# Kernel optimization log

Hardware: AMD Instinct MI355X
Metric: run time of the kernel (lower is better)

Reference implementation:

```python
import jax, jax.numpy as jnp
from jax import lax
import numpy as np

B, N, D = 64, 1025, 384   # tokens = 1 CLS + 32x32 patch grid
G = 32
K = 8                      # num rotation bases
KS = 8                     # num scale bases
R = 8                      # rank of skew bases
H = 128                    # controller hidden dim
CIN = 3 * D                # cls_mean_var pooling
OUT = D
ROT_GATE_BIAS = -4.0
LOCAL_GATE_BIAS = -3.0


def setup_inputs() -> dict:
    key = jax.random.key(0)
    ks = jax.random.split(key, 16)
    f32 = jnp.float32
    inp = {
        "x": jax.random.normal(ks[0], (B, N, D), f32),
        "shared_weight": jax.random.normal(ks[1], (OUT, D), f32) * 0.02,
        "bias": jnp.zeros((OUT,), f32),
        "left_basis": jax.random.normal(ks[2], (K, D, R), f32) * 0.02,
        "right_basis": jax.random.normal(ks[3], (K, D, R), f32) * 0.02,
        "scale_basis": jax.random.normal(ks[4], (KS, OUT), f32) * 0.01,
        "scale_strength": jnp.asarray(0.25, f32),
        "dw_kernel": jax.random.normal(ks[5], (D, 1, 3, 3), f32) * 0.1,  # depthwise 3x3
        "ctrl_w1": jax.random.normal(ks[6], (H, CIN), f32) * 0.02,
        "ctrl_b1": jnp.zeros((H,), f32),
        "w_rot": jax.random.normal(ks[7], (K, H), f32) * 0.02,
        "b_rot": jnp.zeros((K,), f32),
        "w_rgate": jax.random.normal(ks[8], (1, H), f32) * 0.02,
        "b_rgate": jnp.full((1,), ROT_GATE_BIAS, f32),
        "w_lgate": jax.random.normal(ks[9], (1, H), f32) * 0.02,
        "b_lgate": jnp.full((1,), LOCAL_GATE_BIAS, f32),
        "w_scale": jax.random.normal(ks[10], (KS, H), f32) * 0.02,
        "b_scale": jnp.zeros((KS,), f32),
    }
    return inp


def _forward(x, shared_weight, bias, left_basis, right_basis, scale_basis,
             scale_strength, dw_kernel, ctrl_w1, ctrl_b1, w_rot, b_rot,
             w_rgate, b_rgate, w_lgate, b_lgate, w_scale, b_scale):
    b, n, d = x.shape
    # --- conditioning signal: cls | mean | var (unbiased=False) ---
    cls = x[:, 0]
    mean = jnp.mean(x, axis=1)
    var = jnp.var(x, axis=1)
    z = jnp.concatenate([cls, mean, var], axis=-1)          # [B, 3D]
    # --- controller MLP ---
    h = jax.nn.gelu(z @ ctrl_w1.T + ctrl_b1)                 # [B, H]
    rot_coeff = jnp.tanh(h @ w_rot.T + b_rot)                # [B, K]
    rot_gate = jax.nn.sigmoid(h @ w_rgate.T + b_rgate)[:, 0] # [B]
    local_gate = jax.nn.sigmoid(h @ w_lgate.T + b_lgate)[:, 0]
    scale_coeff = jnp.tanh(h @ w_scale.T + b_scale)          # [B, KS]
    # --- gated local depthwise-conv mixer on the patch grid ---
    cls_tok = x[:, :1, :]
    patch = x[:, 1:, :]                                      # [B, G*G, D]
    grid = patch.transpose(0, 2, 1).reshape(b, d, G, G)      # NCHW
    local = lax.conv_general_dilated(
        grid, dw_kernel, window_strides=(1, 1), padding="SAME",
        feature_group_count=d, dimension_numbers=("NCHW", "OIHW", "NCHW"))
    local_tok = local.reshape(b, d, G * G).transpose(0, 2, 1)
    mixed_patch = patch + local_gate[:, None, None] * (local_tok - patch)
    lm = jnp.concatenate([cls_tok, mixed_patch], axis=1)     # [B, N, D]
    # --- normalized skew bases from low-rank factors ---
    basis = (jnp.einsum("kdr,ker->kde", left_basis, right_basis)
             - jnp.einsum("kdr,ker->kde", right_basis, left_basis))  # [K, D, D]
    norm = jnp.maximum(jnp.linalg.norm(basis.reshape(K, -1), axis=1), 1e-6)
    basis = basis / norm[:, None, None]
    # --- per-sample Cayley rotation (fp32 solve) ---
    skew = jnp.einsum("bk,kde->bde", rot_coeff, basis)       # residual_scale = 1.0
    eye = jnp.eye(d, dtype=jnp.float32)
    half = 0.5 * skew
    transform = jnp.linalg.solve(eye - half, jnp.broadcast_to(eye, half.shape) + half)
    transform = transform.astype(x.dtype)
    # --- gated rotation of features ---
    rotated = jnp.einsum("bnd,bdh->bnh", lm, transform)
    mixed = lm + rot_gate[:, None, None] * (rotated - lm)
    # --- shared linear + dynamic output scaling ---
    preact = mixed @ shared_weight.T + bias                  # [B, N, OUT]
    scale_delta = jnp.tanh(scale_coeff @ scale_basis)        # [B, OUT]
    scale = 1.0 + scale_strength * scale_delta[:, None, :]
    return preact * scale


def reference(x, shared_weight, bias, left_basis, right_basis, scale_basis,
              scale_strength, dw_kernel, ctrl_w1, ctrl_b1, w_rot, b_rot,
              w_rgate, b_rgate, w_lgate, b_lgate, w_scale, b_scale):
    return _forward(x, shared_weight, bias, left_basis, right_basis, scale_basis,
                    scale_strength, dw_kernel, ctrl_w1, ctrl_b1, w_rot, b_rot,
                    w_rgate, b_rgate, w_lgate, b_lgate, w_scale, b_scale)
```

## Files before the change

kernel.cpp:

```cpp
#include <hip/hip_runtime.h>
#include <hip/hip_bf16.h>
#include <math.h>

static const int Bb = 64, Nn = 1025, Dd = 384, Kk = 8, Rr = 8, Hh = 128, CINc = 1152, OUTo = 384;

#define OFF_PSTAT 0u
#define OFF_RC    475136u
#define OFF_RG    475648u
#define OFF_LG    475712u
#define OFF_SCALE 476288u
#define OFF_N2    505472u
#define OFF_P     505600u
#define OFF_Q     554752u
#define OFF_G     603904u
#define OFF_QW    620288u
#define OFF_PB    669440u
#define OFF_EP    694016u
#define OFF_ZT    3839744u
#define OFF_WBT   5412608u
#define OFF_LM    10131200u

typedef __attribute__((ext_vector_type(8))) short short8;
typedef __attribute__((ext_vector_type(8))) __bf16 bf16x8;
typedef __attribute__((ext_vector_type(4))) float f32x4;

#define MFMA_BF16(a,b,c) __builtin_amdgcn_mfma_f32_16x16x32_bf16( \
    __builtin_bit_cast(bf16x8,(a)), __builtin_bit_cast(bf16x8,(b)), (c), 0, 0, 0)

#define GLDS16(gp, lp) __builtin_amdgcn_global_load_lds( \
    (__attribute__((address_space(1))) void*)(gp), \
    (__attribute__((address_space(3))) void*)(lp), 16, 0, 0)

__device__ __forceinline__ float gelu_t(float v){
    float u = 0.7978845608028654f*(v + 0.044715f*v*v*v);
    return 0.5f*v*(1.0f + tanhf(u));
}
__device__ __forceinline__ float sigm(float v){ return 1.0f/(1.0f+expf(-v)); }
__device__ __forceinline__ unsigned short f2bf(float v){
    return __builtin_bit_cast(unsigned short, __float2bfloat16(v));
}

__global__ __launch_bounds__(384) void k_statsprep(const float* __restrict__ x,
    const float* __restrict__ lb, const float* __restrict__ rb,
    float* __restrict__ ps, float* __restrict__ n2,
    float* __restrict__ P, float* __restrict__ Q, unsigned short* __restrict__ Pb){
    int bid = blockIdx.x, t = threadIdx.x;
    if (bid < 512){
        int s = bid & 7, b = bid >> 3;
        int dq = t % 96, ng = t / 96;
        int n0 = s*129, n1 = n0+129 < Nn ? n0+129 : Nn;
        const float4* xb = (const float4*)(x + (size_t)b*Nn*Dd);
        float4 sm = make_float4(0.f,0.f,0.f,0.f), sq = make_float4(0.f,0.f,0.f,0.f);
        for (int n = n0+ng; n < n1; n += 4){
            float4 v = xb[(size_t)n*96 + dq];
            sm.x += v.x; sm.y += v.y; sm.z += v.z; sm.w += v.w;
            sq.x += v.x*v.x; sq.y += v.y*v.y; sq.z += v.z*v.z; sq.w += v.w*v.w;
        }
        __shared__ float4 smS[384];
        __shared__ float4 sqS[384];
        smS[t] = sm; sqS[t] = sq;
        __syncthreads();
        if (t < 96){
            float4 a0 = smS[t], a1 = smS[t+96], a2 = smS[t+192], a3 = smS[t+288];
            float4 q0 = sqS[t], q1 = sqS[t+96], q2 = sqS[t+192], q3 = sqS[t+288];
            float4 a = make_float4(a0.x+a1.x+a2.x+a3.x, a0.y+a1.y+a2.y+a3.y, a0.z+a1.z+a2.z+a3.z, a0.w+a1.w+a2.w+a3.w);
            float4 q = make_float4(q0.x+q1.x+q2.x+q3.x, q0.y+q1.y+q2.y+q3.y, q0.z+q1.z+q2.z+q3.z, q0.w+q1.w+q2.w+q3.w);
            ((float4*)(ps + ((size_t)(b*8+s)*2+0)*Dd))[t] = a;
            ((float4*)(ps + ((size_t)(b*8+s)*2+1)*Dd))[t] = q;
        }
    } else if (bid < 520){
        if (t < 64){
            int k = bid - 512;
            int r = t >> 3, s2 = t & 7;
            const float* L = lb + (size_t)k*Dd*Rr;
            const float* R = rb + (size_t)k*Dd*Rr;
            float a = 0.f, bsum = 0.f, c = 0.f, c2 = 0.f;
            for (int d = 0; d < Dd; ++d){
                float lr = L[d*8+r], ls = L[d*8+s2], rr = R[d*8+r], rs = R[d*8+s2];
                a += lr*ls; bsum += rr*rs; c += lr*rs; c2 += ls*rr;
            }
            float contrib = a*bsum - c*c2;
            for (int m = 32; m > 0; m >>= 1) contrib += __shfl_xor(contrib, m, 64);
            if (t == 0) n2[k] = 2.f*contrib;
        }
    } else {
        int idx = (bid - 520)*384 + t;
        int d = idx >> 7, j = idx & 127;
        int k = (j & 63) >> 3, r = j & 7;
        float lv = lb[((size_t)k*Dd + d)*Rr + r];
        float rv = rb[((size_t)k*Dd + d)*Rr + r];
        float pv = (j < 64) ? lv : rv;
        P[idx] = pv;
        Pb[idx] = f2bf(pv);
        Q[idx] = (j < 64) ? rv : lv;
    }
}

__global__ __launch_bounds__(512) void k_ctrlgram(const float* __restrict__ x, const float* __restrict__ ps,
    const float* __restrict__ w1, const float* __restrict__ b1,
    const float* __restrict__ w_rot, const float* __restrict__ b_rot,
    const float* __restrict__ w_rg, const float* __restrict__ b_rg,
    const float* __restrict__ w_lg, const float* __restrict__ b_lg,
    const float* __restrict__ w_sc, const float* __restrict__ b_sc,
    const float* __restrict__ sbasis, const float* __restrict__ sstr,
    const float* __restrict__ P, const float* __restrict__ Q, const float* __restrict__ Wsh,
    float* __restrict__ rc, float* __restrict__ rg, float* __restrict__ lg,
    float* __restrict__ scalev, unsigned short* __restrict__ lm,
    float* __restrict__ G, float* __restrict__ QW){
    int bid = blockIdx.x, t = threadIdx.x;
    if (bid < 128){
        __shared__ float qc[384];
        int i = bid;
        for (int d = t; d < Dd; d += 512) qc[d] = Q[d*128 + i];
        __syncthreads();
        if (t < 128){
            float a = 0.f;
            for (int d = 0; d < Dd; ++d) a += qc[d]*P[d*128 + t];
            G[i*128 + t] = a;
        } else {
            int o = t - 128;
            float a = 0.f;
            const float* wrow = Wsh + (size_t)o*Dd;
            for (int d = 0; d < Dd; ++d) a += qc[d]*wrow[d];
            QW[(size_t)i*OUTo + o] = a;
        }
    } else {
        __shared__ float zs[1152];
        __shared__ float hp[4*128];
        __shared__ float hs[128];
        __shared__ float scl[8];
        int b = bid - 128;
        if (t < 384){
            float sm = 0.f, sq = 0.f;
            for (int s = 0; s < 8; ++s){
                sm += ps[((size_t)(b*8+s)*2+0)*Dd + t];
                sq += ps[((size_t)(b*8+s)*2+1)*Dd + t];
            }
            float mean = sm*(1.0f/Nn);
            float var  = sq*(1.0f/Nn) - mean*mean;
            float cls  = x[(size_t)b*Nn*Dd + t];
            zs[t] = cls; zs[Dd + t] = mean; zs[2*Dd + t] = var;
            lm[(size_t)b*Nn*Dd + t] = f2bf(cls);
        }
        __syncthreads();
        {
            int row = t & 127, part = t >> 7;
            const float* wrow = w1 + (size_t)row*CINc + part*288;
            const float* zp = zs + part*288;
            float acc = 0.f;
            for (int c = 0; c < 288; ++c) acc += zp[c]*wrow[c];
            hp[part*128 + row] = acc;
        }
        __syncthreads();
        if (t < 128)
            hs[t] = gelu_t(hp[t] + hp[128+t] + hp[256+t] + hp[384+t] + b1[t]);
        __syncthreads();
        if (t < 8){
            float acc = b_rot[t]; const float* w = w_rot + (size_t)t*Hh;
            for (int c = 0; c < Hh; ++c) acc += hs[c]*w[c];
            rc[b*8+t] = tanhf(acc);
        } else if (t == 8){
            float acc = b_rg[0];
            for (int c = 0; c < Hh; ++c) acc += hs[c]*w_rg[c];
            rg[b] = sigm(acc);
        } else if (t == 9){
            float acc = b_lg[0];
            for (int c = 0; c < Hh; ++c) acc += hs[c]*w_lg[c];
            lg[b] = sigm(acc);
        } else if (t < 18){
            int q = t-10; float acc = b_sc[q]; const float* w = w_sc + (size_t)q*Hh;
            for (int c = 0; c < Hh; ++c) acc += hs[c]*w[c];
            scl[q] = tanhf(acc);
        }
        __syncthreads();
        if (t < 384){
            float acc = 0.f;
            #pragma unroll
            for (int q = 0; q < 8; ++q) acc += scl[q]*sbasis[q*OUTo + t];
            scalev[(size_t)b*OUTo + t] = 1.0f + sstr[0]*tanhf(acc);
        }
    }
}

__global__ __launch_bounds__(512) void k_cayley(const float* __restrict__ G, const float* __restrict__ rc,
                                                const float* __restrict__ n2, const float* __restrict__ rg,
                                                float* __restrict__ Ep){
    __shared__ float GT[128*128];
    __shared__ float Xs[128*128];
    int b = blockIdx.x, t = threadIdx.x;
    for (int lin = t; lin < 16384; lin += 512){
        int i = lin >> 7, m = lin & 127;
        GT[m*128 + i] = G[lin];
    }
    int j0 = (t & 15)*8, i0 = (t >> 4)*4;
    float dj[8], di[4];
    #pragma unroll
    for (int u = 0; u < 8; ++u){
        int j = j0+u; int k = (j&63)>>3;
        float nrm = fmaxf(sqrtf(n2[k]), 1e-6f);
        float al = 0.5f*rc[b*8+k]/nrm;
        dj[u] = (j < 64) ? al : -al;
    }
    #pragma unroll
    for (int u = 0; u < 4; ++u){
        int i = i0+u; int k = (i&63)>>3;
        float nrm = fmaxf(sqrtf(n2[k]), 1e-6f);
        float al = 0.5f*rc[b*8+k]/nrm;
        di[u] = (i < 64) ? al : -al;
    }
    __syncthreads();
    float B0[4][8], acc[4][8];
    #pragma unroll
    for (int ui = 0; ui < 4; ++ui)
        #pragma unroll
        for (int uj = 0; uj < 8; ++uj){
            int i = i0+ui, j = j0+uj;
            float g = GT[j*128 + i];
            B0[ui][uj] = di[ui]*g*dj[uj] + ((i==j) ? di[ui] : 0.f);
        }
    #pragma unroll
    for (int ui = 0; ui < 4; ++ui)
        #pragma unroll
        for (int uj = 0; uj < 8; ++uj)
            Xs[(i0+ui)*128 + j0+uj] = B0[ui][uj];
    __syncthreads();
    for (int pass = 0; pass < 2; ++pass){
        #pragma unroll
        for (int ui = 0; ui < 4; ++ui)
            #pragma unroll
            for (int uj = 0; uj < 8; ++uj) acc[ui][uj] = 0.f;
        for (int m = 0; m < 128; ++m){
            float4 g4 = *(const float4*)&GT[m*128 + i0];
            float4 xa = *(const float4*)&Xs[m*128 + j0];
            float4 xb = *(const float4*)&Xs[m*128 + j0 + 4];
            float gi[4] = {g4.x, g4.y, g4.z, g4.w};
            float xv[8] = {xa.x, xa.y, xa.z, xa.w, xb.x, xb.y, xb.z, xb.w};
            #pragma unroll
            for (int ui = 0; ui < 4; ++ui)
                #pragma unroll
                for (int uj = 0; uj < 8; ++uj)
                    acc[ui][uj] += gi[ui]*xv[uj];
        }
        if (pass == 0){
            __syncthreads();
            #pragma unroll
            for (int ui = 0; ui < 4; ++ui)
                #pragma unroll
                for (int uj = 0; uj < 8; ++uj)
                    Xs[(i0+ui)*128 + j0+uj] = B0[ui][uj] + di[ui]*acc[ui][uj];
            __syncthreads();
        }
    }
    float rgb = rg[b];
    #pragma unroll
    for (int ui = 0; ui < 4; ++ui){
        int i = i0+ui;
        float o[8];
        #pragma unroll
        for (int uj = 0; uj < 8; ++uj){
            int j = j0+uj;
            float x2 = B0[ui][uj] + di[ui]*acc[ui][uj];
            o[uj] = rgb*(x2 + ((i==j) ? di[ui] : 0.f));
        }
        float4* ep4 = (float4*)(Ep + ((size_t)b*128 + i)*128 + j0);
        ep4[0] = make_float4(o[0], o[1], o[2], o[3]);
        ep4[1] = make_float4(o[4], o[5], o[6], o[7]);
    }
}

__global__ __launch_bounds__(384) void k_zmlm(const float* __restrict__ x, const float* __restrict__ kw,
    const float* __restrict__ lg, const float* __restrict__ Ep, const float* __restrict__ QW,
    unsigned short* __restrict__ lm, unsigned short* __restrict__ ZT){
    int bid = blockIdx.x, t = threadIdx.x;
    if (bid < 2048){
        __shared__ float kws[9*384];
        int flat = bid;
        int work = (flat & 7)*256 + (flat >> 3);
        int b = work >> 5, gy = work & 31;
        for (int i = t; i < 3456; i += 384){
            int d = i % 384, tap = i / 384;
            kws[tap*384 + d] = kw[d*9 + tap];
        }
        __syncthreads();
        int dq = t % 96, gxg = t / 96;
        float lgb = lg[b];
        const float4* xb = (const float4*)(x + (size_t)b*Nn*Dd);
        unsigned short* lmb = lm + (size_t)b*Nn*Dd;
        #pragma unroll
        for (int u = 0; u < 8; ++u){
            int gx = gxg + 4*u;
            int n = 1 + (gy << 5) + gx;
            float4 xc = xb[(size_t)n*96 + dq];
            float ax = 0.f, ay = 0.f, az = 0.f, aw = 0.f;
            #pragma unroll
            for (int ky = 0; ky < 3; ++ky){
                int yy = gy + ky - 1;
                if ((unsigned)yy < 32u){
                    #pragma unroll
                    for (int kx = 0; kx < 3; ++kx){
                        int xx = gx + kx - 1;
                        if ((unsigned)xx < 32u){
                            float4 xv = xb[(size_t)(1 + (yy << 5) + xx)*96 + dq];
                            const float4 kv = *(const float4*)(&kws[(ky*3+kx)*384 + dq*4]);
                            ax += xv.x*kv.x; ay += xv.y*kv.y; az += xv.z*kv.z; aw += xv.w*kv.w;
                        }
                    }
                }
            }
            ushort4 o4;
            o4.x = f2bf(xc.x + lgb*(ax - xc.x));
            o4.y = f2bf(xc.y + lgb*(ay - xc.y));
            o4.z = f2bf(xc.z + lgb*(az - xc.z));
            o4.w = f2bf(xc.w + lgb*(aw - xc.w));
            *(ushort4*)(lmb + (size_t)n*Dd + dq*4) = o4;
        }
    } else {
        __shared__ float Es[4*128];
        int z = bid - 2048;
        int ig = z & 31, b = z >> 5;
        int i0 = ig*4;
        for (int lin = t; lin < 512; lin += 384)
            Es[lin] = Ep[((size_t)b*128 + i0 + (lin >> 7))*128 + (lin & 127)];
        __syncthreads();
        float a0=0.f, a1=0.f, a2=0.f, a3=0.f;
        for (int m = 0; m < 128; ++m){
            float qw = QW[(size_t)m*OUTo + t];
            a0 += Es[m]*qw; a1 += Es[128+m]*qw; a2 += Es[256+m]*qw; a3 += Es[384+m]*qw;
        }
        ushort4 uv;
        uv.x = f2bf(a0); uv.y = f2bf(a1); uv.z = f2bf(a2); uv.w = f2bf(a3);
        *(ushort4*)(ZT + ((size_t)b*OUTo + t)*128 + i0) = uv;
    }
}

__global__ __launch_bounds__(256) void k_wbt(const unsigned short* __restrict__ ZT, const unsigned short* __restrict__ Pb,
                                             const float* __restrict__ Wsh, unsigned short* __restrict__ WbT){
    __shared__ short8 As[256];
    __shared__ short8 Bs[256];
    int b = blockIdx.y;
    int mt = blockIdx.x/6, nt2 = blockIdx.x%6;
    int m0 = mt*64, n0 = nt2*64;
    int t = threadIdx.x;
    int w = t>>6, l = t&63;
    int wr = w>>1, wc = w&1;
    const unsigned short* Ab = ZT + (size_t)b*OUTo*128;
    int lrow = t>>2, lseg = t&3;
    f32x4 acc[2][2];
    #pragma unroll
    for (int mi=0;mi<2;++mi)
        #pragma unroll
        for (int ni=0;ni<2;++ni)
            #pragma unroll
            for (int q=0;q<4;++q) acc[mi][ni][q] = 0.f;
    for (int kt = 0; kt < 4; ++kt){
        int k0 = kt*32;
        short8 av = *(const short8*)(Ab + (size_t)(m0+lrow)*128 + k0 + lseg*8);
        short8 bv = *(const short8*)(Pb + (size_t)(n0+lrow)*128 + k0 + lseg*8);
        __syncthreads();
        As[lseg*64 + lrow] = av;
        Bs[lseg*64 + lrow] = bv;
        __syncthreads();
        short8 a0 = As[(l>>4)*64 + wr*32 + (l&15)];
        short8 a1 = As[(l>>4)*64 + wr*32 + 16 + (l&15)];
        short8 b0 = Bs[(l>>4)*64 + wc*32 + (l&15)];
        short8 b1 = Bs[(l>>4)*64 + wc*32 + 16 + (l&15)];
        acc[0][0] = MFMA_BF16(a0, b0, acc[0][0]);
        acc[0][1] = MFMA_BF16(a0, b1, acc[0][1]);
        acc[1][0] = MFMA_BF16(a1, b0, acc[1][0]);
        acc[1][1] = MFMA_BF16(a1, b1, acc[1][1]);
    }
    unsigned short* Wo = WbT + (size_t)b*OUTo*Dd;
    #pragma unroll
    for (int mi=0;mi<2;++mi){
        #pragma unroll
        for (int ni=0;ni<2;++ni){
            int col = n0 + wc*32 + ni*16 + (l&15);
            #pragma unroll
            for (int r=0;r<4;++r){
                int row = m0 + wr*32 + mi*16 + (l>>4)*4 + r;
                float v = Wsh[(size_t)row*Dd + col] + acc[mi][ni][r];
                Wo[(size_t)row*Dd + col] = f2bf(v);
            }
        }
    }
}

__global__ __launch_bounds__(256) void k_gemm_nt(const unsigned short* __restrict__ lm, const unsigned short* __restrict__ WbT,
                                                 const float* __restrict__ bias, const float* __restrict__ scalev,
                                                 float* __restrict__ out){
    __shared__ unsigned short smem[32768];
    __shared__ float svs[128];
    __shared__ float bvs[128];
    int flat = blockIdx.x;
    int work = (flat & 7)*216 + (flat >> 3);
    int b = work / 27;
    int r = work - b*27;
    int nt = r / 3, ot = r - nt*3;
    int n0 = nt*128, o0 = ot*128;
    int t = threadIdx.x;
    int w = t >> 6, l = t & 63;
    int wr = w >> 1, wc = w & 1;
    const unsigned short* Ab = lm + (size_t)b*Nn*Dd;
    const unsigned short* Bt = WbT + (size_t)b*OUTo*Dd;
    if (t < 128){ svs[t] = scalev[(size_t)b*OUTo + o0 + t]; bvs[t] = bias[o0 + t]; }
    int srow = l >> 2;
    int gch  = (l & 3) ^ ((l >> 3) & 3);
    f32x4 acc[4][4];
    #pragma unroll
    for (int fi = 0; fi < 4; ++fi)
        #pragma unroll
        for (int fj = 0; fj < 4; ++fj)
            #pragma unroll
            for (int q = 0; q < 4; ++q) acc[fi][fj][q] = 0.f;

#define STG(bufi, k0) { \
    unsigned short* Adst = &smem[(bufi)*8192 + (w*32)*32]; \
    unsigned short* Bdst = &smem[(bufi)*8192 + 4096 + (w*32)*32]; \
    GLDS16(Ab + (size_t)(n0 + w*32 + srow)*Dd + (k0) + gch*8, Adst); \
    GLDS16(Ab + (size_t)(n0 + w*32 + 16 + srow)*Dd + (k0) + gch*8, Adst + 512); \
    GLDS16(Bt + (size_t)(o0 + w*32 + srow)*Dd + (k0) + gch*8, Bdst); \
    GLDS16(Bt + (size_t)(o0 + w*32 + 16 + srow)*Dd + (k0) + gch*8, Bdst + 512); }

    STG(0, 0);
    STG(1, 32);
    int rch = ((l>>4) ^ (((l&15)>>1)&3)) * 8;
    int raBase = (wr*64 + (l&15))*32;
    int rbBase = (wc*64 + (l&15))*32;
    for (int kt = 0; kt < 12; ++kt){
        if (kt < 10) STG((kt+2)&3, (kt+2)*32);
        if (kt < 10)       asm volatile("s_waitcnt vmcnt(8)" ::: "memory");
        else if (kt == 10) asm volatile("s_waitcnt vmcnt(4)" ::: "memory");
        else               asm volatile("s_waitcnt vmcnt(0)" ::: "memory");
        __builtin_amdgcn_s_barrier();
        __builtin_amdgcn_sched_barrier(0);
        const unsigned short* As  = &smem[(kt&3)*8192];
        const unsigned short* Bs2 = &smem[(kt&3)*8192 + 4096];
        short8 a[4], bb[4];
        #pragma unroll
        for (int f = 0; f < 4; ++f){
            a[f]  = *(const short8*)&As [raBase + f*512 + rch];
            bb[f] = *(const short8*)&Bs2[rbBase + f*512 + rch];
        }
        #pragma unroll
        for (int fi = 0; fi < 4; ++fi)
            #pragma unroll
            for (int fj = 0; fj < 4; ++fj)
                acc[fi][fj] = MFMA_BF16(a[fi], bb[fj], acc[fi][fj]);
    }
#undef STG
    float* Cs = (float*)smem;
    #pragma unroll
    for (int h = 0; h < 2; ++h){
        __syncthreads();
        if (wr == h){
            #pragma unroll
            for (int fi = 0; fi < 4; ++fi)
                #pragma unroll
                for (int fj = 0; fj < 4; ++fj){
                    int col = wc*64 + fj*16 + (l&15);
                    #pragma unroll
                    for (int q = 0; q < 4; ++q){
                        int row = fi*16 + (l>>4)*4 + q;
                        Cs[row*132 + col] = acc[fi][fj][q];
                    }
                }
        }
        __syncthreads();
        #pragma unroll
        for (int p = 0; p < 8; ++p){
            int idx = p*256 + t;
            int row = idx >> 5, c4 = idx & 31;
            int gr = n0 + h*64 + row;
            if (gr < Nn){
                float4 v = *(const float4*)&Cs[row*132 + c4*4];
                float4 o4;
                o4.x = svs[c4*4+0]*(bvs[c4*4+0] + v.x);
                o4.y = svs[c4*4+1]*(bvs[c4*4+1] + v.y);
                o4.z = svs[c4*4+2]*(bvs[c4*4+2] + v.z);
                o4.w = svs[c4*4+3]*(bvs[c4*4+3] + v.w);
                *(float4*)(out + ((size_t)b*Nn + gr)*OUTo + o0 + c4*4) = o4;
            }
        }
    }
}

extern "C" void kernel_launch(void* const* d_in, const int* in_sizes, int n_in,
                              void* d_out, int out_size, void* d_ws, size_t ws_size,
                              hipStream_t stream){
    const float* x     = (const float*)d_in[0];
    const float* Wsh   = (const float*)d_in[1];
    const float* bias  = (const float*)d_in[2];
    const float* lb    = (const float*)d_in[3];
    const float* rb    = (const float*)d_in[4];
    const float* sbasis= (const float*)d_in[5];
    const float* sstr  = (const float*)d_in[6];
    const float* kw    = (const float*)d_in[7];
    const float* w1    = (const float*)d_in[8];
    const float* b1    = (const float*)d_in[9];
    const float* w_rot = (const float*)d_in[10];
    const float* b_rot = (const float*)d_in[11];
    const float* w_rg  = (const float*)d_in[12];
    const float* b_rg  = (const float*)d_in[13];
    const float* w_lg  = (const float*)d_in[14];
    const float* b_lg  = (const float*)d_in[15];
    const float* w_sc  = (const float*)d_in[16];
    const float* b_sc  = (const float*)d_in[17];
    float* out = (float*)d_out;
    float* ws  = (float*)d_ws;

    float* ps     = ws + OFF_PSTAT;
    float* rc     = ws + OFF_RC;
    float* rg     = ws + OFF_RG;
    float* lg     = ws + OFF_LG;
    float* scalev = ws + OFF_SCALE;
    float* n2     = ws + OFF_N2;
    float* P      = ws + OFF_P;
    float* Q      = ws + OFF_Q;
    float* G      = ws + OFF_G;
    float* QW     = ws + OFF_QW;
    unsigned short* Pb  = (unsigned short*)(ws + OFF_PB);
    float* Ep     = ws + OFF_EP;
    unsigned short* ZT  = (unsigned short*)(ws + OFF_ZT);
    unsigned short* WbT = (unsigned short*)(ws + OFF_WBT);
    unsigned short* lmb = (unsigned short*)(ws + OFF_LM);

    k_statsprep<<<648, 384, 0, stream>>>(x, lb, rb, ps, n2, P, Q, Pb);
    k_ctrlgram <<<192, 512, 0, stream>>>(x, ps, w1, b1, w_rot, b_rot, w_rg, b_rg, w_lg, b_lg,
                                         w_sc, b_sc, sbasis, sstr, P, Q, Wsh,
                                         rc, rg, lg, scalev, lmb, G, QW);
    k_cayley   <<<Bb, 512, 0, stream>>>(G, rc, n2, rg, Ep);
    k_zmlm     <<<4096, 384, 0, stream>>>(x, kw, lg, Ep, QW, lmb, ZT);
    k_wbt      <<<dim3(36, Bb), 256, 0, stream>>>(ZT, Pb, Wsh, WbT);
    k_gemm_nt  <<<1728, 256, 0, stream>>>(lmb, WbT, bias, scalev, out);
}
```

Baseline: 224.3 us.

## Stage depthwise-conv halo rows in LDS and split channels across blocks

The depthwise 3x3 conv branch of k_zmlm now loads a 3-row by 34-column halo tile for half of the channels into shared memory, with zero padding, and reads all nine taps from LDS. Before, every tap was a bounds-checked global load. Kernel weights are held in registers instead of shared memory, and each block covers one row and one channel half, so the grid doubles from 2048 to 4096 conv blocks. The aim is to replace repeated global/L2 traffic with LDS reuse, at the cost of about 78KB of shared memory per block, which may reduce occupancy.

```diff
diff --git a/kernel.cpp b/kernel.cpp
--- a/kernel.cpp
+++ b/kernel.cpp
@@ -271,52 +271,61 @@
 __global__ __launch_bounds__(384) void k_zmlm(const float* __restrict__ x, const float* __restrict__ kw,
     const float* __restrict__ lg, const float* __restrict__ Ep, const float* __restrict__ QW,
     unsigned short* __restrict__ lm, unsigned short* __restrict__ ZT){
+    __shared__ float4 xs4[4896];
     int bid = blockIdx.x, t = threadIdx.x;
-    if (bid < 2048){
-        __shared__ float kws[9*384];
-        int flat = bid;
-        int work = (flat & 7)*256 + (flat >> 3);
-        int b = work >> 5, gy = work & 31;
-        for (int i = t; i < 3456; i += 384){
-            int d = i % 384, tap = i / 384;
-            kws[tap*384 + d] = kw[d*9 + tap];
-        }
-        __syncthreads();
-        int dq = t % 96, gxg = t / 96;
+    if (bid < 4096){
+        int work = (bid & 7)*512 + (bid >> 3);
+        int b = work >> 6, sub = work & 63;
+        int gy = sub >> 1, dhalf = sub & 1;
+        int dq = t % 48, gxg = t / 48;
+        const float4* xb4 = (const float4*)(x + (size_t)b*Nn*Dd);
+        int based = dhalf*192 + dq*4;
+        float4 kvr[9];
+        #pragma unroll
+        for (int tap = 0; tap < 9; ++tap)
+            kvr[tap] = make_float4(kw[(based+0)*9+tap], kw[(based+1)*9+tap],
+                                   kw[(based+2)*9+tap], kw[(based+3)*9+tap]);
+        #pragma unroll
+        for (int i = 0; i < 13; ++i){
+            int lin = i*384 + t;
+            if (lin < 4896){
+                int r = lin / 1632;
+                int rem = lin - r*1632;
+                int xxp = rem / 48, c = rem - xxp*48;
+                int yy = gy + r - 1, xx = xxp - 1;
+                float4 v = make_float4(0.f,0.f,0.f,0.f);
+                if ((unsigned)yy < 32u && (unsigned)xx < 32u)
+                    v = xb4[(size_t)(1 + (yy << 5) + xx)*96 + dhalf*48 + c];
+                xs4[lin] = v;
+            }
+        }
+        __syncthreads();
         float lgb = lg[b];
-        const float4* xb = (const float4*)(x + (size_t)b*Nn*Dd);
         unsigned short* lmb = lm + (size_t)b*Nn*Dd;
         #pragma unroll
-        for (int u = 0; u < 8; ++u){
-            int gx = gxg + 4*u;
+        for (int u = 0; u < 4; ++u){
+            int gx = gxg*4 + u;
+            float4 xc = xs4[(34 + gx+1)*48 + dq];
+            float ax = 0.f, ay = 0.f, az = 0.f, aw = 0.f;
+            #pragma unroll
+            for (int ky = 0; ky < 3; ++ky)
+                #pragma unroll
+                for (int kx = 0; kx < 3; ++kx){
+                    float4 xv = xs4[(ky*34 + gx+kx)*48 + dq];
+                    float4 kv = kvr[ky*3+kx];
+                    ax += xv.x*kv.x; ay += xv.y*kv.y; az += xv.z*kv.z; aw += xv.w*kv.w;
+                }
             int n = 1 + (gy << 5) + gx;
-            float4 xc = xb[(size_t)n*96 + dq];
-            float ax = 0.f, ay = 0.f, az = 0.f, aw = 0.f;
-            #pragma unroll
-            for (int ky = 0; ky < 3; ++ky){
-                int yy = gy + ky - 1;
-                if ((unsigned)yy < 32u){
-                    #pragma unroll
-                    for (int kx = 0; kx < 3; ++kx){
-                        int xx = gx + kx - 1;
-                        if ((unsigned)xx < 32u){
-                            float4 xv = xb[(size_t)(1 + (yy << 5) + xx)*96 + dq];
-                            const float4 kv = *(const float4*)(&kws[(ky*3+kx)*384 + dq*4]);
-                            ax += xv.x*kv.x; ay += xv.y*kv.y; az += xv.z*kv.z; aw += xv.w*kv.w;
-                        }
-                    }
-                }
-            }
             ushort4 o4;
             o4.x = f2bf(xc.x + lgb*(ax - xc.x));
             o4.y = f2bf(xc.y + lgb*(ay - xc.y));
             o4.z = f2bf(xc.z + lgb*(az - xc.z));
             o4.w = f2bf(xc.w + lgb*(aw - xc.w));
-            *(ushort4*)(lmb + (size_t)n*Dd + dq*4) = o4;
+            *(ushort4*)(lmb + (size_t)n*Dd + based) = o4;
         }
     } else {
-        __shared__ float Es[4*128];
-        int z = bid - 2048;
+        float* Es = (float*)xs4;
+        int z = bid - 4096;
         int ig = z & 31, b = z >> 5;
         int i0 = ig*4;
         for (int lin = t; lin < 512; lin += 384)
@@ -529,7 +538,7 @@
                                          w_sc, b_sc, sbasis, sstr, P, Q, Wsh,
                                          rc, rg, lg, scalev, lmb, G, QW);
     k_cayley   <<<Bb, 512, 0, stream>>>(G, rc, n2, rg, Ep);
-    k_zmlm     <<<4096, 384, 0, stream>>>(x, kw, lg, Ep, QW, lmb, ZT);
+    k_zmlm     <<<6144, 384, 0, stream>>>(x, kw, lg, Ep, QW, lmb, ZT);
     k_wbt      <<<dim3(36, Bb), 256, 0, stream>>>(ZT, Pb, Wsh, WbT);
     k_gemm_nt  <<<1728, 256, 0, stream>>>(lmb, WbT, bias, scalev, out);
 }
```

After: 261.7 us. 16.7% more time.
